# Kernel optimization log

Hardware: AMD Instinct MI355X
Metric: run time of the kernel (lower is better)

The kernel has to match this reference:

```python
import jax, jax.numpy as jnp
import numpy as np

B, S, D, H = 4, 2048, 1024, 16
DK = D // H

def setup_inputs() -> dict:
    key = jax.random.key(0)
    ks = jax.random.split(key, 8)
    q = jax.random.normal(ks[0], (B, S, D), dtype=jnp.float32)
    k = jax.random.normal(ks[1], (B, S, D), dtype=jnp.float32)
    v = jax.random.normal(ks[2], (B, S, D), dtype=jnp.float32)
    # broadcastable causal mask [1,1,S,S]; 0 -> masked
    mask = jnp.tril(jnp.ones((S, S), dtype=jnp.int32))[None, None]
    sc = 1.0 / np.sqrt(D)
    w_q = jax.random.normal(ks[3], (D, D), dtype=jnp.float32) * sc
    w_k = jax.random.normal(ks[4], (D, D), dtype=jnp.float32) * sc
    w_v = jax.random.normal(ks[5], (D, D), dtype=jnp.float32) * sc
    w_o = jax.random.normal(ks[6], (D, D), dtype=jnp.float32) * sc
    return {"q": q, "k": k, "v": v, "mask": mask,
            "w_q": w_q, "w_k": w_k, "w_v": w_v, "w_o": w_o}


def reference(q, k, v, mask, w_q, w_k, w_v, w_o):
    # Linear (no bias): x @ W^T, torch convention
    def proj(x, w):
        return jnp.einsum('bsd,ed->bse', x, w)
    # [B,S,D] -> [B,H,S,DK]
    def split_heads(x):
        return x.reshape(B, S, H, DK).transpose(0, 2, 1, 3)

    query = split_heads(proj(q, w_q))
    key_ = split_heads(proj(k, w_k))
    value = split_heads(proj(v, w_v))

    scores = jnp.einsum('bhqd,bhkd->bhqk', query, key_) / jnp.sqrt(
        jnp.asarray(DK, dtype=query.dtype))
    scores = jnp.where(mask == 0, jnp.asarray(-1e9, dtype=scores.dtype), scores)
    attn = jax.nn.softmax(scores, axis=-1)  # dropout p=0.0 -> identity
    x = jnp.einsum('bhqk,bhkd->bhqd', attn, value)
    x = x.transpose(0, 2, 1, 3).reshape(B, S, D)
    return jnp.einsum('bsd,ed->bse', x, w_o)
```

## Files before the change

### kernel.cpp

```cpp
#include <hip/hip_runtime.h>
#include <hip/hip_bf16.h>

#define B_ 4
#define S_ 2048
#define D_ 1024
#define H_ 16
#define DK_ 64

typedef unsigned short u16;
typedef __bf16 bf16x8 __attribute__((ext_vector_type(8)));
typedef float f32x4 __attribute__((ext_vector_type(4)));

typedef const unsigned int __attribute__((address_space(1))) guint;
typedef unsigned int __attribute__((address_space(3))) luint;

__device__ __forceinline__ void gld16(const u16* g, u16* l) {
  __builtin_amdgcn_global_load_lds((guint*)g, (luint*)l, 16, 0, 0);
}

__device__ __forceinline__ u16 f2b(float f) {
  __hip_bfloat16 h = __float2bfloat16(f);
  return __builtin_bit_cast(u16, h);
}
__device__ __forceinline__ ushort4 f2b4(float4 f) {
  ushort4 r;
  r.x = f2b(f.x); r.y = f2b(f.y); r.z = f2b(f.z); r.w = f2b(f.w);
  return r;
}
__device__ __forceinline__ bf16x8 ldb8(const u16* p) {
  union { uint4 u; bf16x8 v; } x;
  x.u = *(const uint4*)p;
  return x.v;
}

struct CvtAllArgs {
  const float* s[7];
  u16* d[7];
};
__global__ __launch_bounds__(256) void cvt_all(CvtAllArgs a) {
  const int z = blockIdx.y;
  const int bx = blockIdx.x;
  const float* s;
  u16* d;
  int i;
  if (z < 3) {
    s = a.s[z]; d = a.d[z];
    i = bx * 256 + threadIdx.x;
  } else {
    if (bx >= 2048) return;
    const int wsel = bx >> 9;
    s = a.s[3 + wsel]; d = a.d[3 + wsel];
    i = (bx & 511) * 256 + threadIdx.x;
  }
  float4 x = ((const float4*)s)[2 * i];
  float4 y = ((const float4*)s)[2 * i + 1];
  ((ushort4*)d)[2 * i] = f2b4(x);
  ((ushort4*)d)[2 * i + 1] = f2b4(y);
}

template <bool OUT_QKV>
__device__ __forceinline__ void gemm_body(const u16* __restrict__ A,
                                          const u16* __restrict__ W,
                                          void* __restrict__ C, float scale) {
  constexpr int K = D_;
  __shared__ u16 As[128 * 32];
  __shared__ u16 Ws[128 * 32];
  const int t = threadIdx.x;
  const int lane = t & 63, w = t >> 6;
  const int quad = lane >> 4, m16 = lane & 15;
  const int bn = blockIdx.x, bm = blockIdx.y;
  const int wm = (w >> 1) * 64, wn = (w & 1) * 64;
  const int sr = lane >> 2, sc8 = (lane & 3) * 8;

  f32x4 acc[4][4];
  const f32x4 zero = {0.f, 0.f, 0.f, 0.f};
#pragma unroll
  for (int i = 0; i < 4; i++)
#pragma unroll
    for (int j = 0; j < 4; j++) acc[i][j] = zero;

  const u16* Ag = A + (size_t)(bm * 128 + w * 32 + sr) * K + sc8;
  const u16* Wg = W + (size_t)(bn * 128 + w * 32 + sr) * K + sc8;
  u16* AsB = &As[w * 1024];
  u16* WsB = &Ws[w * 1024];

  for (int k0 = 0; k0 < K; k0 += 32) {
    __syncthreads();
    gld16(Ag + k0, AsB);
    gld16(Ag + (size_t)16 * K + k0, AsB + 512);
    gld16(Wg + k0, WsB);
    gld16(Wg + (size_t)16 * K + k0, WsB + 512);
    __syncthreads();

    bf16x8 af[4], wf[4];
#pragma unroll
    for (int mt = 0; mt < 4; mt++)
      af[mt] = ldb8(&As[(wm + mt * 16 + m16) * 32 + quad * 8]);
#pragma unroll
    for (int nt = 0; nt < 4; nt++)
      wf[nt] = ldb8(&Ws[(wn + nt * 16 + m16) * 32 + quad * 8]);
#pragma unroll
    for (int mt = 0; mt < 4; mt++)
#pragma unroll
      for (int nt = 0; nt < 4; nt++)
        acc[mt][nt] = __builtin_amdgcn_mfma_f32_16x16x32_bf16(af[mt], wf[nt],
                                                              acc[mt][nt], 0, 0, 0);
  }

#pragma unroll
  for (int mt = 0; mt < 4; mt++) {
#pragma unroll
    for (int r = 0; r < 4; r++) {
      int m = bm * 128 + wm + mt * 16 + quad * 4 + r;
#pragma unroll
      for (int nt = 0; nt < 4; nt++) {
        int n = bn * 128 + wn + nt * 16 + m16;
        float val = acc[mt][nt][r] * scale;
        if (OUT_QKV) {
          int b = m >> 11, s = m & (S_ - 1);
          int h = n >> 6, dk = n & 63;
          ((u16*)C)[(((size_t)b * H_ + h) * S_ + s) * DK_ + dk] = f2b(val);
        } else {
          ((float*)C)[(size_t)m * D_ + n] = val;
        }
      }
    }
  }
}

struct GemmQkvArgs {
  const u16 *a0, *a1, *a2;
  const u16 *w0, *w1, *w2;
  u16 *c0, *c1, *c2;
  float qscale;
};
__global__ __launch_bounds__(256) void gemm_qkv(GemmQkvArgs g) {
  const int z = blockIdx.z;
  const u16* A = z == 0 ? g.a0 : z == 1 ? g.a1 : g.a2;
  const u16* W = z == 0 ? g.w0 : z == 1 ? g.w1 : g.w2;
  u16* C = z == 0 ? g.c0 : z == 1 ? g.c1 : g.c2;
  gemm_body<true>(A, W, C, z == 0 ? g.qscale : 1.0f);
}

__global__ __launch_bounds__(256) void gemm_o(const u16* __restrict__ A,
                                              const u16* __restrict__ W,
                                              float* __restrict__ C) {
  gemm_body<false>(A, W, C, 1.0f);
}

__global__ __launch_bounds__(256) void transpose_v(const u16* __restrict__ Vp,
                                                   u16* __restrict__ VpT) {
  constexpr int LDT = 72;
  __shared__ u16 T[64 * LDT];
  const int t = threadIdx.x;
  const int s0 = blockIdx.x * 64, bh = blockIdx.y;
  const size_t base = (size_t)bh * S_ * DK_;
  const int rot = t & 7;
#pragma unroll
  for (int i = 0; i < 2; i++) {
    int c = t + i * 256, row = c >> 3, c8 = (c & 7) * 8;
    union { uint4 u; u16 s[8]; } uv;
    uv.u = *(const uint4*)(Vp + base + (size_t)(s0 + row) * DK_ + c8);
#pragma unroll
    for (int j0 = 0; j0 < 8; j0++) {
      int j = (j0 + rot) & 7;
      T[(c8 + j) * LDT + row] = uv.s[j];
    }
  }
  __syncthreads();
#pragma unroll
  for (int i = 0; i < 2; i++) {
    int c = t + i * 256, row = c >> 3, c8 = (c & 7) * 8;
    uint4 val = *(const uint4*)&T[row * LDT + c8];
    *(uint4*)(VpT + base + (size_t)row * S_ + s0 + c8) = val;
  }
}

__global__ __launch_bounds__(512, 4) void flash_attn(const u16* __restrict__ Qp,
                                                     const u16* __restrict__ Kp,
                                                     const u16* __restrict__ VpT,
                                                     u16* __restrict__ Xb) {
  constexpr int LDK = 72;
  __shared__ u16 Ks[2][64 * LDK];
  __shared__ u16 Vt[2][64 * LDK];
  __shared__ u16 Ps[8][16 * LDK];
  const int t = threadIdx.x;
  const int lane = t & 63, w = t >> 6;
  const int quad = lane >> 4, m16 = lane & 15;
  const int id = blockIdx.x;
  const int g = (id >> 3) & 7;
  const int bh = (id & 7) * 8 + (id >> 6);
  const int b = bh >> 4, h = bh & (H_ - 1);
  const size_t base = (size_t)bh * S_ * DK_;
  const int srow = t >> 3, sc8 = (t & 7) * 8;
  const f32x4 zero = {0.f, 0.f, 0.f, 0.f};

#pragma unroll 1
  for (int pi = 0; pi < 2; pi++) {
    const int qt = pi ? (15 - g) : g;
    const int q0 = qt * 128;
    const int nT = 2 * qt + 2;

    const int qrow = q0 + w * 16 + m16;
    bf16x8 qf0 = ldb8(Qp + base + (size_t)qrow * DK_ + quad * 8);
    bf16x8 qf1 = ldb8(Qp + base + (size_t)qrow * DK_ + 32 + quad * 8);

    f32x4 acc[4];
#pragma unroll
    for (int i = 0; i < 4; i++) acc[i] = zero;
    float rsum[4] = {0.f, 0.f, 0.f, 0.f};

    uint4 kr = *(const uint4*)(Kp + base + (size_t)srow * DK_ + sc8);
    uint4 vr = *(const uint4*)(VpT + base + (size_t)srow * S_ + sc8);

#pragma unroll 1
    for (int ti = 0; ti < nT; ti++) {
      const int kt0 = ti * 64;
      const int cur = ti & 1;
      *(uint4*)&Ks[cur][srow * LDK + sc8] = kr;
      *(uint4*)&Vt[cur][srow * LDK + sc8] = vr;
      __syncthreads();
      if (ti + 1 < nT) {
        kr = *(const uint4*)(Kp + base + (size_t)(kt0 + 64 + srow) * DK_ + sc8);
        vr = *(const uint4*)(VpT + base + (size_t)srow * S_ + kt0 + 64 + sc8);
      }
      const u16* Kc = Ks[cur];
      const u16* Vc = Vt[cur];

      f32x4 sc[4];
      __builtin_amdgcn_s_setprio(1);
#pragma unroll
      for (int nt = 0; nt < 4; nt++) {
        bf16x8 kf0 = ldb8(&Kc[(nt * 16 + m16) * LDK + quad * 8]);
        bf16x8 kf1 = ldb8(&Kc[(nt * 16 + m16) * LDK + 32 + quad * 8]);
        sc[nt] = __builtin_amdgcn_mfma_f32_16x16x32_bf16(qf0, kf0, zero, 0, 0, 0);
        sc[nt] = __builtin_amdgcn_mfma_f32_16x16x32_bf16(qf1, kf1, sc[nt], 0, 0, 0);
      }
      __builtin_amdgcn_s_setprio(0);

      if (ti >= nT - 2) {
        const int rbase = q0 + w * 16 + quad * 4;
#pragma unroll
        for (int nt = 0; nt < 4; nt++) {
          int kg = kt0 + nt * 16 + m16;
#pragma unroll
          for (int r = 0; r < 4; r++)
            if (kg > rbase + r) sc[nt][r] = -1e30f;
        }
      }

      u16* Pw = &Ps[w][0];
#pragma unroll
      for (int nt = 0; nt < 4; nt++)
#pragma unroll
        for (int r = 0; r < 4; r++) {
          float p = __builtin_amdgcn_exp2f(sc[nt][r]);
          rsum[r] += p;
          Pw[(quad * 4 + r) * LDK + nt * 16 + m16] = f2b(p);
        }

      __builtin_amdgcn_s_setprio(1);
#pragma unroll
      for (int s2 = 0; s2 < 2; s2++) {
        bf16x8 pf = ldb8(&Pw[m16 * LDK + s2 * 32 + quad * 8]);
#pragma unroll
        for (int nt = 0; nt < 4; nt++) {
          bf16x8 vf = ldb8(&Vc[(nt * 16 + m16) * LDK + s2 * 32 + quad * 8]);
          acc[nt] = __builtin_amdgcn_mfma_f32_16x16x32_bf16(pf, vf, acc[nt], 0, 0, 0);
        }
      }
      __builtin_amdgcn_s_setprio(0);
    }

    float rcv[4];
#pragma unroll
    for (int r = 0; r < 4; r++) {
      float x = rsum[r];
#pragma unroll
      for (int off = 1; off < 16; off <<= 1) x += __shfl_xor(x, off, 16);
      rcv[r] = __builtin_amdgcn_rcpf(x);
    }
#pragma unroll
    for (int nt = 0; nt < 4; nt++)
#pragma unroll
      for (int r = 0; r < 4; r++) {
        int rg = q0 + w * 16 + quad * 4 + r;
        Xb[((size_t)b * S_ + rg) * D_ + h * DK_ + nt * 16 + m16] =
            f2b(acc[nt][r] * rcv[r]);
      }
  }
}

extern "C" void kernel_launch(void* const* d_in, const int* in_sizes, int n_in,
                              void* d_out, int out_size, void* d_ws, size_t ws_size,
                              hipStream_t stream) {
  (void)in_sizes; (void)n_in; (void)out_size; (void)ws_size;
  const float* q = (const float*)d_in[0];
  const float* k = (const float*)d_in[1];
  const float* v = (const float*)d_in[2];
  const float* wq = (const float*)d_in[4];
  const float* wk = (const float*)d_in[5];
  const float* wv = (const float*)d_in[6];
  const float* wo = (const float*)d_in[7];

  const size_t nBSD = (size_t)B_ * S_ * D_;
  const size_t nDD = (size_t)D_ * D_;
  u16* ab = (u16*)d_ws;
  u16* wqb = ab + nBSD;
  u16* wkb = wqb + nDD;
  u16* wvb = wkb + nDD;
  u16* wob = wvb + nDD;
  u16* Qp = wob + nDD;
  u16* Kp = Qp + nBSD;
  u16* Vp = Kp + nBSD;
  u16* VpT = ab;
  u16* Xb = Vp;
  u16* abk = (u16*)d_out;
  u16* abv = abk + nBSD;

  const float qscale = 0.125f * 1.44269504089f;

  CvtAllArgs ca = {{q, k, v, wq, wk, wv, wo}, {ab, abk, abv, wqb, wkb, wvb, wob}};
  cvt_all<<<dim3(nBSD / 2048, 4), 256, 0, stream>>>(ca);

  GemmQkvArgs gq = {ab, abk, abv, wqb, wkb, wvb, Qp, Kp, Vp, qscale};
  gemm_qkv<<<dim3(D_ / 128, (B_ * S_) / 128, 3), 256, 0, stream>>>(gq);

  transpose_v<<<dim3(S_ / 64, B_ * H_), 256, 0, stream>>>(Vp, VpT);
  flash_attn<<<512, 512, 0, stream>>>(Qp, Kp, VpT, Xb);

  gemm_o<<<dim3(D_ / 128, (B_ * S_) / 128), 256, 0, stream>>>(Xb, wob, (float*)d_out);
}
```

Baseline: 359.1 us.

## Fuse fp32-to-bf16 activation conversion into QKV GEMM and swizzle block order

Result: faster. 343.3 us (-4.4%).

```diff
diff --git a/kernel.cpp b/kernel.cpp
--- a/kernel.cpp
+++ b/kernel.cpp
@@ -33,42 +33,133 @@
   return x.v;
 }
 
-struct CvtAllArgs {
-  const float* s[7];
-  u16* d[7];
+struct Cvt4Args {
+  const float *s0, *s1, *s2, *s3;
+  u16 *d0, *d1, *d2, *d3;
 };
-__global__ __launch_bounds__(256) void cvt_all(CvtAllArgs a) {
-  const int z = blockIdx.y;
-  const int bx = blockIdx.x;
-  const float* s;
-  u16* d;
-  int i;
-  if (z < 3) {
-    s = a.s[z]; d = a.d[z];
-    i = bx * 256 + threadIdx.x;
-  } else {
-    if (bx >= 2048) return;
-    const int wsel = bx >> 9;
-    s = a.s[3 + wsel]; d = a.d[3 + wsel];
-    i = (bx & 511) * 256 + threadIdx.x;
-  }
+__global__ __launch_bounds__(256) void cvt4_bf16(Cvt4Args a) {
+  int z = blockIdx.y;
+  const float* s = z == 0 ? a.s0 : z == 1 ? a.s1 : z == 2 ? a.s2 : a.s3;
+  u16* d = z == 0 ? a.d0 : z == 1 ? a.d1 : z == 2 ? a.d2 : a.d3;
+  int i = blockIdx.x * 256 + threadIdx.x;
   float4 x = ((const float4*)s)[2 * i];
   float4 y = ((const float4*)s)[2 * i + 1];
   ((ushort4*)d)[2 * i] = f2b4(x);
   ((ushort4*)d)[2 * i + 1] = f2b4(y);
 }
 
-template <bool OUT_QKV>
-__device__ __forceinline__ void gemm_body(const u16* __restrict__ A,
-                                          const u16* __restrict__ W,
-                                          void* __restrict__ C, float scale) {
+__device__ __forceinline__ void swz_bnbm(int& bn, int& bm) {
+  const int id2 = blockIdx.y * 8 + blockIdx.x;
+  const int wg = (id2 & 7) * 64 + (id2 >> 3);
+  bn = wg & 7;
+  bm = wg >> 3;
+}
+
+__device__ __forceinline__ void gemm_body_qkv(const float* __restrict__ A,
+                                              const u16* __restrict__ W,
+                                              u16* __restrict__ C, float scale) {
   constexpr int K = D_;
   __shared__ u16 As[128 * 32];
   __shared__ u16 Ws[128 * 32];
   const int t = threadIdx.x;
   const int lane = t & 63, w = t >> 6;
   const int quad = lane >> 4, m16 = lane & 15;
-  const int bn = blockIdx.x, bm = blockIdx.y;
+  int bn, bm;
+  swz_bnbm(bn, bm);
+  const int wm = (w >> 1) * 64, wn = (w & 1) * 64;
+  const int sr = lane >> 2, sc8 = (lane & 3) * 8;
+
+  f32x4 acc[4][4];
+  const f32x4 zero = {0.f, 0.f, 0.f, 0.f};
+#pragma unroll
+  for (int i = 0; i < 4; i++)
+#pragma unroll
+    for (int j = 0; j < 4; j++) acc[i][j] = zero;
+
+  const float* Ag = A + (size_t)(bm * 128 + w * 32 + sr) * K + sc8;
+  const u16* Wg = W + (size_t)(bn * 128 + w * 32 + sr) * K + sc8;
+  u16* AsB = &As[w * 1024];
+  u16* WsB = &Ws[w * 1024];
+
+  float4 ar0 = *(const float4*)(Ag);
+  float4 ar1 = *(const float4*)(Ag + 4);
+  float4 ar2 = *(const float4*)(Ag + (size_t)16 * K);
+  float4 ar3 = *(const float4*)(Ag + (size_t)16 * K + 4);
+
+  for (int k0 = 0; k0 < K; k0 += 32) {
+    __syncthreads();
+    union { ushort4 s4[2]; uint4 u; } lo, hi;
+    lo.s4[0] = f2b4(ar0); lo.s4[1] = f2b4(ar1);
+    hi.s4[0] = f2b4(ar2); hi.s4[1] = f2b4(ar3);
+    *(uint4*)&AsB[sr * 32 + sc8] = lo.u;
+    *(uint4*)&AsB[512 + sr * 32 + sc8] = hi.u;
+    gld16(Wg + k0, WsB);
+    gld16(Wg + (size_t)16 * K + k0, WsB + 512);
+    __syncthreads();
+    if (k0 + 32 < K) {
+      ar0 = *(const float4*)(Ag + k0 + 32);
+      ar1 = *(const float4*)(Ag + k0 + 36);
+      ar2 = *(const float4*)(Ag + (size_t)16 * K + k0 + 32);
+      ar3 = *(const float4*)(Ag + (size_t)16 * K + k0 + 36);
+    }
+
+    bf16x8 af[4], wf[4];
+#pragma unroll
+    for (int mt = 0; mt < 4; mt++)
+      af[mt] = ldb8(&As[(wm + mt * 16 + m16) * 32 + quad * 8]);
+#pragma unroll
+    for (int nt = 0; nt < 4; nt++)
+      wf[nt] = ldb8(&Ws[(wn + nt * 16 + m16) * 32 + quad * 8]);
+#pragma unroll
+    for (int mt = 0; mt < 4; mt++)
+#pragma unroll
+      for (int nt = 0; nt < 4; nt++)
+        acc[mt][nt] = __builtin_amdgcn_mfma_f32_16x16x32_bf16(af[mt], wf[nt],
+                                                              acc[mt][nt], 0, 0, 0);
+  }
+
+#pragma unroll
+  for (int mt = 0; mt < 4; mt++) {
+#pragma unroll
+    for (int r = 0; r < 4; r++) {
+      int m = bm * 128 + wm + mt * 16 + quad * 4 + r;
+#pragma unroll
+      for (int nt = 0; nt < 4; nt++) {
+        int n = bn * 128 + wn + nt * 16 + m16;
+        float val = acc[mt][nt][r] * scale;
+        int b = m >> 11, s = m & (S_ - 1);
+        int h = n >> 6, dk = n & 63;
+        C[(((size_t)b * H_ + h) * S_ + s) * DK_ + dk] = f2b(val);
+      }
+    }
+  }
+}
+
+struct GemmQkvArgs {
+  const float *a0, *a1, *a2;
+  const u16 *w0, *w1, *w2;
+  u16 *c0, *c1, *c2;
+  float qscale;
+};
+__global__ __launch_bounds__(256) void gemm_qkv(GemmQkvArgs g) {
+  const int z = blockIdx.z;
+  const float* A = z == 0 ? g.a0 : z == 1 ? g.a1 : g.a2;
+  const u16* W = z == 0 ? g.w0 : z == 1 ? g.w1 : g.w2;
+  u16* C = z == 0 ? g.c0 : z == 1 ? g.c1 : g.c2;
+  gemm_body_qkv(A, W, C, z == 0 ? g.qscale : 1.0f);
+}
+
+__global__ __launch_bounds__(256) void gemm_o(const u16* __restrict__ A,
+                                              const u16* __restrict__ W,
+                                              float* __restrict__ C) {
+  constexpr int K = D_;
+  __shared__ u16 As[128 * 32];
+  __shared__ u16 Ws[128 * 32];
+  const int t = threadIdx.x;
+  const int lane = t & 63, w = t >> 6;
+  const int quad = lane >> 4, m16 = lane & 15;
+  int bn, bm;
+  swz_bnbm(bn, bm);
   const int wm = (w >> 1) * 64, wn = (w & 1) * 64;
   const int sr = lane >> 2, sc8 = (lane & 3) * 8;
 
@@ -115,37 +206,10 @@
 #pragma unroll
       for (int nt = 0; nt < 4; nt++) {
         int n = bn * 128 + wn + nt * 16 + m16;
-        float val = acc[mt][nt][r] * scale;
-        if (OUT_QKV) {
-          int b = m >> 11, s = m & (S_ - 1);
-          int h = n >> 6, dk = n & 63;
-          ((u16*)C)[(((size_t)b * H_ + h) * S_ + s) * DK_ + dk] = f2b(val);
-        } else {
-          ((float*)C)[(size_t)m * D_ + n] = val;
-        }
-      }
-    }
-  }
-}
-
-struct GemmQkvArgs {
-  const u16 *a0, *a1, *a2;
-  const u16 *w0, *w1, *w2;
-  u16 *c0, *c1, *c2;
-  float qscale;
-};
-__global__ __launch_bounds__(256) void gemm_qkv(GemmQkvArgs g) {
-  const int z = blockIdx.z;
-  const u16* A = z == 0 ? g.a0 : z == 1 ? g.a1 : g.a2;
-  const u16* W = z == 0 ? g.w0 : z == 1 ? g.w1 : g.w2;
-  u16* C = z == 0 ? g.c0 : z == 1 ? g.c1 : g.c2;
-  gemm_body<true>(A, W, C, z == 0 ? g.qscale : 1.0f);
-}
-
-__global__ __launch_bounds__(256) void gemm_o(const u16* __restrict__ A,
-                                              const u16* __restrict__ W,
-                                              float* __restrict__ C) {
-  gemm_body<false>(A, W, C, 1.0f);
+        C[(size_t)m * D_ + n] = acc[mt][nt][r];
+      }
+    }
+  }
 }
 
 __global__ __launch_bounds__(256) void transpose_v(const u16* __restrict__ Vp,
@@ -305,25 +369,22 @@
 
   const size_t nBSD = (size_t)B_ * S_ * D_;
   const size_t nDD = (size_t)D_ * D_;
-  u16* ab = (u16*)d_ws;
-  u16* wqb = ab + nBSD;
+  u16* VpT = (u16*)d_ws;
+  u16* wqb = VpT + nBSD;
   u16* wkb = wqb + nDD;
   u16* wvb = wkb + nDD;
   u16* wob = wvb + nDD;
   u16* Qp = wob + nDD;
   u16* Kp = Qp + nBSD;
   u16* Vp = Kp + nBSD;
-  u16* VpT = ab;
   u16* Xb = Vp;
-  u16* abk = (u16*)d_out;
-  u16* abv = abk + nBSD;
 
   const float qscale = 0.125f * 1.44269504089f;
 
-  CvtAllArgs ca = {{q, k, v, wq, wk, wv, wo}, {ab, abk, abv, wqb, wkb, wvb, wob}};
-  cvt_all<<<dim3(nBSD / 2048, 4), 256, 0, stream>>>(ca);
-
-  GemmQkvArgs gq = {ab, abk, abv, wqb, wkb, wvb, Qp, Kp, Vp, qscale};
+  Cvt4Args wargs = {wq, wk, wv, wo, wqb, wkb, wvb, wob};
+  cvt4_bf16<<<dim3(nDD / 2048, 4), 256, 0, stream>>>(wargs);
+
+  GemmQkvArgs gq = {q, k, v, wqb, wkb, wvb, Qp, Kp, Vp, qscale};
   gemm_qkv<<<dim3(D_ / 128, (B_ * S_) / 128, 3), 256, 0, stream>>>(gq);
 
   transpose_v<<<dim3(S_ / 64, B_ * H_), 256, 0, stream>>>(Vp, VpT);
```
